# Kernel optimization log

Measured on AMD Instinct MI355X. Metric: run time of the kernel, lower is better.

The kernel has to match this reference:

```python
import jax, jax.numpy as jnp
import numpy as np

B, S, D, E, H, TOPK = 4, 2048, 1024, 32, 128, 4

def setup_inputs() -> dict:
    key = jax.random.key(0)
    k1, k2, k3, k4 = jax.random.split(key, 4)
    x = jax.random.normal(k1, (B, S, D), jnp.float32)
    expert_sel = jax.random.normal(k2, (E, D), jnp.float32) * (D ** -0.5)
    keys = jax.random.normal(k3, (E, D, H), jnp.float32) * (D ** -0.5)
    values = jax.random.normal(k4, (E, H, D), jnp.float32) * (H ** -0.5)
    return {"x": x, "expert_sel": expert_sel, "keys": keys, "values": values, "n_heads": TOPK}

def reference(x, expert_sel, keys, values, n_heads):
    # x: [B,S,D]; expert_sel: [E,D]; keys: [E,D,H]; values: [E,H,D]
    Bv, Sv, Dv = x.shape
    Ev = keys.shape[0]
    xf = x.reshape(-1, Dv)                                  # [N,D]
    N = xf.shape[0]
    gate = jax.nn.sigmoid(xf @ expert_sel.T)                # [N,E] sigmoid gating (sigma-MoE)
    vals, idx = jax.lax.top_k(gate, n_heads)                # [N,k] selected experts + gate weights
    # dense per-token-per-expert gate weights; zero for non-selected experts
    g = jnp.zeros((N, Ev), x.dtype).at[jnp.arange(N)[:, None], idx].set(vals)  # [N,E]
    # grouped expert FFN, expressed densely over the (small) expert axis:
    # out = sum_e g[n,e] * relu(x @ keys[e]) @ values[e]
    h = jax.nn.relu(jnp.einsum('nd,edh->enh', xf, keys))    # [E,N,H]
    out = jnp.einsum('enh,ehd->nd', h * g.T[:, :, None], values)  # [N,D]
    return out.reshape(Bv, Sv, Dv)
```

## Files before the change

### kernel.cpp

```cpp
#include <hip/hip_runtime.h>
#include <hip/hip_bf16.h>

#define NTOK 8192
#define DDIM 1024
#define NEXP 32
#define HDIM 128
#define TOPK 4

typedef __attribute__((ext_vector_type(8))) short bf16x8;
typedef __attribute__((ext_vector_type(4))) float f32x4;

typedef unsigned int uint_g __attribute__((address_space(1)));
typedef unsigned int uint_l __attribute__((address_space(3)));

__device__ __forceinline__ void async_cp16(const void* g, void* l) {
    __builtin_amdgcn_global_load_lds((const uint_g*)g, (uint_l*)l, 16, 0, 0);
}

__device__ inline unsigned short f2bf(float f) {
    unsigned int u = __builtin_bit_cast(unsigned int, f);
    unsigned int r = (u + 0x7fffu + ((u >> 16) & 1u)) >> 16;
    return (unsigned short)r;
}
__device__ inline float bf2f(unsigned short s) {
    unsigned int u = ((unsigned int)s) << 16;
    return __builtin_bit_cast(float, u);
}

__global__ __launch_bounds__(256) void prep_gate(
    const float* __restrict__ x, const float* __restrict__ es,
    const float* __restrict__ keys, const float* __restrict__ values,
    unsigned short* __restrict__ Kb, unsigned short* __restrict__ Vb,
    unsigned short* __restrict__ Xb,
    int* __restrict__ cnt, int* __restrict__ tok_list, float* __restrict__ gates)
{
    const int tid = threadIdx.x;

    if (blockIdx.x >= 512) {
        int idx = (int)(blockIdx.x - 512) * 256 + tid;
        unsigned short o[8];
        if (idx < NEXP * 128 * 128) {
            int n = idx & 127, k0 = (idx >> 7) & 127, e = idx >> 14;
            const float* s = keys + ((size_t)e * DDIM + k0 * 8) * HDIM + n;
            #pragma unroll
            for (int j = 0; j < 8; ++j) o[j] = f2bf(s[(size_t)j * HDIM]);
            *(uint4*)&Kb[(size_t)idx * 8] = *(uint4*)o;
        } else {
            idx -= NEXP * 128 * 128;
            int n = idx & 1023, k0 = (idx >> 10) & 15, e = idx >> 14;
            const float* s = values + ((size_t)e * HDIM + k0 * 8) * DDIM + n;
            #pragma unroll
            for (int j = 0; j < 8; ++j) o[j] = f2bf(s[(size_t)j * DDIM]);
            *(uint4*)&Vb[(size_t)idx * 8] = *(uint4*)o;
        }
        return;
    }

    const int n0 = (int)blockIdx.x * 16;

    __shared__ float smem[4608];
    __shared__ float Ls[16 * 33];
    __shared__ int hist[NEXP];
    __shared__ int bbase[NEXP];
    float* Xt  = smem;
    float* Est = smem + 64 * 36;
    float* Lp  = smem;

    const int t4  = (tid & 3) * 4;
    const int e4  = ((tid >> 2) & 7) * 4;
    const int rep = tid >> 5;

    const int xr = tid & 15, xc4 = (tid >> 4) * 4;
    const int er = tid & 31, ec8 = (tid >> 5) * 8;

    const int ctok = tid >> 4, cd4 = (tid & 15) * 4;

    const int rtok = tid >> 5, re = tid & 31;

    float lsum[2] = {0.f, 0.f};

    if (tid < NEXP) hist[tid] = 0;

    float4 xv  = *(const float4*)&x[(size_t)(n0 + xr) * DDIM + xc4];
    float4 ev0 = *(const float4*)&es[(size_t)er * DDIM + ec8];
    float4 ev1 = *(const float4*)&es[(size_t)er * DDIM + ec8 + 4];

    for (int q = 0; q < 4; ++q) {
        float acc[4][4] = {};

        for (int dci = 0; dci < 4; ++dci) {
            const int dc = q * 256 + dci * 64;
            __syncthreads();
            {
                Xt[(xc4 + 0) * 36 + xr] = xv.x; Xt[(xc4 + 1) * 36 + xr] = xv.y;
                Xt[(xc4 + 2) * 36 + xr] = xv.z; Xt[(xc4 + 3) * 36 + xr] = xv.w;
                Est[(ec8 + 0) * 36 + er] = ev0.x; Est[(ec8 + 1) * 36 + er] = ev0.y;
                Est[(ec8 + 2) * 36 + er] = ev0.z; Est[(ec8 + 3) * 36 + er] = ev0.w;
                Est[(ec8 + 4) * 36 + er] = ev1.x; Est[(ec8 + 5) * 36 + er] = ev1.y;
                Est[(ec8 + 6) * 36 + er] = ev1.z; Est[(ec8 + 7) * 36 + er] = ev1.w;
            }
            const int nxt = dc + 64;
            if (nxt < DDIM) {
                xv  = *(const float4*)&x[(size_t)(n0 + xr) * DDIM + nxt + xc4];
                ev0 = *(const float4*)&es[(size_t)er * DDIM + nxt + ec8];
                ev1 = *(const float4*)&es[(size_t)er * DDIM + nxt + ec8 + 4];
            }
            __syncthreads();

            {
                unsigned short o[4];
                #pragma unroll
                for (int j = 0; j < 4; ++j) o[j] = f2bf(Xt[(cd4 + j) * 36 + ctok]);
                *(uint2*)&Xb[(size_t)(n0 + ctok) * DDIM + dc + cd4] = *(uint2*)o;
            }

            #pragma unroll
            for (int s = 0; s < 8; ++s) {
                int d = s * 8 + rep;
                float4 xa4 = *(const float4*)&Xt[d * 36 + t4];
                float4 ea4 = *(const float4*)&Est[d * 36 + e4];
                const float xa[4] = {xa4.x, xa4.y, xa4.z, xa4.w};
                const float ea[4] = {ea4.x, ea4.y, ea4.z, ea4.w};
                #pragma unroll
                for (int i = 0; i < 4; ++i)
                    #pragma unroll
                    for (int j = 0; j < 4; ++j)
                        acc[i][j] = fmaf(xa[i], ea[j], acc[i][j]);
            }
        }

        __syncthreads();
        #pragma unroll
        for (int i = 0; i < 4; ++i)
            #pragma unroll
            for (int j = 0; j < 4; ++j)
                Lp[(rep * 16 + t4 + i) * 33 + e4 + j] = acc[i][j];
        __syncthreads();

        #pragma unroll
        for (int h = 0; h < 2; ++h) {
            int tok = rtok + h * 8;
            float s = 0.f;
            #pragma unroll
            for (int r = 0; r < 8; ++r) s += Lp[(r * 16 + tok) * 33 + re];
            lsum[h] += s;
        }
    }

    #pragma unroll
    for (int h = 0; h < 2; ++h) Ls[(rtok + h * 8) * 33 + re] = lsum[h];
    __syncthreads();

    int sel[TOPK]; int lpos[TOPK];
    if (tid < 16) {
        float lg[NEXP];
        #pragma unroll
        for (int e2 = 0; e2 < NEXP; ++e2) lg[e2] = Ls[tid * 33 + e2];
        float sv[TOPK];
        #pragma unroll
        for (int j = 0; j < TOPK; ++j) {
            float bv = -3.0e38f; int bi = 0;
            #pragma unroll
            for (int e2 = 0; e2 < NEXP; ++e2) {
                bool taken = false;
                #pragma unroll
                for (int qq = 0; qq < j; ++qq) taken = taken || (sel[qq] == e2);
                float v = taken ? -3.0e38f : lg[e2];
                if (v > bv) { bv = v; bi = e2; }
            }
            sel[j] = bi; sv[j] = bv;
        }
        #pragma unroll
        for (int j = 0; j < TOPK; ++j) {
            gates[(size_t)(n0 + tid) * TOPK + j] = 1.f / (1.f + expf(-sv[j]));
            lpos[j] = atomicAdd(&hist[sel[j]], 1);
        }
    }
    __syncthreads();
    if (tid < NEXP) bbase[tid] = atomicAdd(&cnt[tid], hist[tid]);
    __syncthreads();
    if (tid < 16) {
        #pragma unroll
        for (int j = 0; j < TOPK; ++j)
            tok_list[(size_t)sel[j] * NTOK + bbase[sel[j]] + lpos[j]] = (n0 + tid) * TOPK + j;
    }
}

__global__ __launch_bounds__(256) void ffn_fused(
    const unsigned short* __restrict__ Xb,
    const unsigned short* __restrict__ Kb,
    const unsigned short* __restrict__ Vb,
    const int* __restrict__ cnt, const int* __restrict__ tok_list,
    const float* __restrict__ gates,
    unsigned short* __restrict__ Ob)
{
    const int bid = blockIdx.x;
    const int e = bid & 31, tile = bid >> 5;
    const int c = cnt[e], base = tile * 32;
    if (base >= c) return;
    const int nt   = min(32, c - base);
    const int tid  = threadIdx.x, wave = tid >> 6, lane = tid & 63;
    const int lm   = lane & 15, quad = lane >> 4;
    const int r2   = (wave >> 1) * 16;
    const int c2   = (wave & 1) * 64;
    const int cw   = (wave & 1) * 32;

    __shared__ __align__(16) unsigned short KV[8192];
    __shared__ __align__(16) unsigned short XO[2304];
    __shared__ __align__(16) unsigned short Hs[32 * 140];
    __shared__ int slot[32]; __shared__ int gtok[32]; __shared__ float gs[32];

    if (tid < 32) {
        if (tid < nt) {
            int v = tok_list[(size_t)e * NTOK + base + tid];
            slot[tid] = v; gtok[tid] = v >> 2; gs[tid] = gates[v];
        } else { slot[tid] = -1; gtok[tid] = 0; gs[tid] = 0.f; }
    }
    __syncthreads();

    const unsigned short* Ke = Kb + (size_t)e * 131072;
    const unsigned short* Ve = Vb + (size_t)e * 131072;
    const unsigned short* xrowb = Xb + (size_t)gtok[lane & 31] * DDIM + (lane >> 5) * 8;

    f32x4 acc[4];
    #pragma unroll
    for (int j = 0; j < 4; ++j) acc[j] = (f32x4){0.f, 0.f, 0.f, 0.f};

    auto stageA = [&](int t) {
        int dc = t * 64;
        #pragma unroll
        for (int i = 0; i < 4; ++i) {
            int p = wave * 4 + i;
            async_cp16(Ke + ((size_t)(dc / 8 + (p >> 1)) * 128 + (p & 1) * 64 + lane) * 8,
                       &KV[p * 512]);
        }
        async_cp16(xrowb + dc + wave * 16, &XO[wave * 512]);
    };

    stageA(0);
    __syncthreads();

    for (int t = 0; t < 16; ++t) {
        #pragma unroll
        for (int ks = 0; ks < 2; ++ks) {
            int k0 = ks * 4 + quad;
            bf16x8 a0 = *(const bf16x8*)&XO[(k0 * 32 + r2 + lm) * 8];
            #pragma unroll
            for (int tj = 0; tj < 4; ++tj) {
                bf16x8 bb = *(const bf16x8*)&KV[(k0 * 128 + c2 + tj * 16 + lm) * 8];
                acc[tj] = __builtin_amdgcn_mfma_f32_16x16x32_bf16(a0, bb, acc[tj], 0, 0, 0);
            }
        }
        if (t < 15) {
            __syncthreads();
            stageA(t + 1);
            __syncthreads();
        }
    }

    #pragma unroll
    for (int reg = 0; reg < 4; ++reg) {
        int m = r2 + quad * 4 + reg;
        float g = gs[m];
        #pragma unroll
        for (int tj = 0; tj < 4; ++tj)
            Hs[m * 140 + c2 + tj * 16 + lm] = f2bf(fmaxf(acc[tj][reg], 0.f) * g);
    }
    __syncthreads();

    auto stageV = [&](int cc) {
        #pragma unroll
        for (int i = 0; i < 4; ++i) {
            int p = wave * 4 + i;
            async_cp16(Ve + ((size_t)p * 1024 + cc * 64 + lane) * 8, &KV[p * 512]);
        }
    };

    stageV(0);
    __syncthreads();

    bf16x8 hf[4];
    #pragma unroll
    for (int ks = 0; ks < 4; ++ks)
        hf[ks] = *(const bf16x8*)&Hs[(r2 + lm) * 140 + (ks * 4 + quad) * 8];

    const int om = tid >> 3, oq = tid & 7;
    const int os = slot[om];

    for (int cc = 0; cc < 16; ++cc) {
        f32x4 acc2[2];
        acc2[0] = (f32x4){0.f, 0.f, 0.f, 0.f};
        acc2[1] = (f32x4){0.f, 0.f, 0.f, 0.f};

        #pragma unroll
        for (int ks = 0; ks < 4; ++ks) {
            int k0 = ks * 4 + quad;
            #pragma unroll
            for (int tj = 0; tj < 2; ++tj) {
                bf16x8 bb = *(const bf16x8*)&KV[(k0 * 64 + cw + tj * 16 + lm) * 8];
                acc2[tj] = __builtin_amdgcn_mfma_f32_16x16x32_bf16(hf[ks], bb, acc2[tj], 0, 0, 0);
            }
        }

        #pragma unroll
        for (int reg = 0; reg < 4; ++reg) {
            int m = r2 + quad * 4 + reg;
            XO[m * 72 + cw + lm]      = f2bf(acc2[0][reg]);
            XO[m * 72 + cw + 16 + lm] = f2bf(acc2[1][reg]);
        }
        __syncthreads();

        if (os >= 0) {
            uint4 v0 = *(const uint4*)&XO[om * 72 + oq * 8];
            *(uint4*)(Ob + (size_t)os * DDIM + cc * 64 + oq * 8) = v0;
        }
        if (cc < 15) stageV(cc + 1);
        __syncthreads();
    }
}

__global__ __launch_bounds__(256) void reduce_out(
    const unsigned short* __restrict__ Ob, float* __restrict__ out)
{
    const int tid = threadIdx.x;
    const int n   = blockIdx.x * 2 + (tid >> 7);
    const int cc  = (tid & 127) * 8;

    float s[8] = {};
    #pragma unroll
    for (int j = 0; j < 4; ++j) {
        uint4 v = *(const uint4*)&Ob[((size_t)n * 4 + j) * DDIM + cc];
        const unsigned int w[4] = {v.x, v.y, v.z, v.w};
        #pragma unroll
        for (int q = 0; q < 4; ++q) {
            s[q * 2 + 0] += bf2f((unsigned short)(w[q] & 0xffff));
            s[q * 2 + 1] += bf2f((unsigned short)(w[q] >> 16));
        }
    }
    float4 o0 = {s[0], s[1], s[2], s[3]};
    float4 o1 = {s[4], s[5], s[6], s[7]};
    *(float4*)&out[(size_t)n * DDIM + cc]     = o0;
    *(float4*)&out[(size_t)n * DDIM + cc + 4] = o1;
}

extern "C" void kernel_launch(void* const* d_in, const int* in_sizes, int n_in,
                              void* d_out, int out_size, void* d_ws, size_t ws_size,
                              hipStream_t stream) {
    const float* x      = (const float*)d_in[0];
    const float* es     = (const float*)d_in[1];
    const float* keys   = (const float*)d_in[2];
    const float* values = (const float*)d_in[3];
    float* out          = (float*)d_out;

    char* w = (char*)d_ws;
    int*   cnt      = (int*)w;               w += 256;
    int*   tok_list = (int*)w;               w += (size_t)NEXP * NTOK * sizeof(int);
    float* gates    = (float*)w;             w += (size_t)NTOK * TOPK * sizeof(float);
    unsigned short* Kb = (unsigned short*)w; w += (size_t)NEXP * 128 * 128 * 8 * 2;
    unsigned short* Vb = (unsigned short*)w; w += (size_t)NEXP * 16 * 1024 * 8 * 2;
    unsigned short* Xb = (unsigned short*)w; w += (size_t)NTOK * DDIM * 2;
    unsigned short* Ob = (unsigned short*)w;

    hipMemsetAsync(cnt, 0, NEXP * sizeof(int), stream);

    prep_gate<<<512 + 4096, 256, 0, stream>>>(x, es, keys, values, Kb, Vb, Xb,
                                              cnt, tok_list, gates);
    ffn_fused<<<256 * NEXP, 256, 0, stream>>>(Xb, Kb, Vb, cnt, tok_list, gates, Ob);
    reduce_out<<<NTOK / 2, 256, 0, stream>>>(Ob, out);
}
```

Baseline: 197.1 us.

## Double-buffer K/V tiles in LDS and load X rows directly into registers

The K and V weight tiles now go into two LDS buffers, with prefetch issued two steps ahead. This drops one of the two barriers per iteration in both GEMM loops. X activations are read straight from global memory into registers with one-step prefetch instead of being staged through LDS. The output staging buffer is also double-buffered so the next tile's writes do not race the global stores. The aim is to overlap global loads with MFMA work, at the cost of roughly doubling LDS usage, which may reduce how many blocks fit per CU.

```diff
diff --git a/kernel.cpp b/kernel.cpp
--- a/kernel.cpp
+++ b/kernel.cpp
@@ -205,9 +205,9 @@
     const int c2   = (wave & 1) * 64;
     const int cw   = (wave & 1) * 32;
 
-    __shared__ __align__(16) unsigned short KV[8192];
-    __shared__ __align__(16) unsigned short XO[2304];
+    __shared__ __align__(16) unsigned short KV[2][8192];
     __shared__ __align__(16) unsigned short Hs[32 * 140];
+    __shared__ __align__(16) unsigned short OSB[2][2304];
     __shared__ int slot[32]; __shared__ int gtok[32]; __shared__ float gs[32];
 
     if (tid < 32) {
@@ -220,44 +220,58 @@
 
     const unsigned short* Ke = Kb + (size_t)e * 131072;
     const unsigned short* Ve = Vb + (size_t)e * 131072;
-    const unsigned short* xrowb = Xb + (size_t)gtok[lane & 31] * DDIM + (lane >> 5) * 8;
-
-    f32x4 acc[4];
-    #pragma unroll
-    for (int j = 0; j < 4; ++j) acc[j] = (f32x4){0.f, 0.f, 0.f, 0.f};
-
-    auto stageA = [&](int t) {
-        int dc = t * 64;
+    const unsigned short* xp = Xb + (size_t)gtok[r2 + lm] * DDIM + quad * 8;
+
+    auto stageK = [&](int t, int cb) {
         #pragma unroll
         for (int i = 0; i < 4; ++i) {
             int p = wave * 4 + i;
-            async_cp16(Ke + ((size_t)(dc / 8 + (p >> 1)) * 128 + (p & 1) * 64 + lane) * 8,
-                       &KV[p * 512]);
-        }
-        async_cp16(xrowb + dc + wave * 16, &XO[wave * 512]);
+            async_cp16(Ke + ((size_t)(t * 8 + (p >> 1)) * 128 + (p & 1) * 64 + lane) * 8,
+                       &KV[cb][p * 512]);
+        }
     };
-
-    stageA(0);
+    auto stageV = [&](int cc, int vb) {
+        #pragma unroll
+        for (int i = 0; i < 4; ++i) {
+            int p = wave * 4 + i;
+            async_cp16(Ve + ((size_t)p * 1024 + cc * 64 + lane) * 8, &KV[vb][p * 512]);
+        }
+    };
+
+    f32x4 acc[4];
+    #pragma unroll
+    for (int j = 0; j < 4; ++j) acc[j] = (f32x4){0.f, 0.f, 0.f, 0.f};
+
+    stageK(0, 0);
+    stageK(1, 1);
+    bf16x8 xc0 = *(const bf16x8*)&xp[0];
+    bf16x8 xc1 = *(const bf16x8*)&xp[32];
     __syncthreads();
 
     for (int t = 0; t < 16; ++t) {
+        bf16x8 xn0, xn1;
+        if (t < 15) {
+            xn0 = *(const bf16x8*)&xp[(t + 1) * 64];
+            xn1 = *(const bf16x8*)&xp[(t + 1) * 64 + 32];
+        }
+        const unsigned short* B = KV[t & 1];
         #pragma unroll
         for (int ks = 0; ks < 2; ++ks) {
             int k0 = ks * 4 + quad;
-            bf16x8 a0 = *(const bf16x8*)&XO[(k0 * 32 + r2 + lm) * 8];
+            bf16x8 a0 = ks ? xc1 : xc0;
             #pragma unroll
             for (int tj = 0; tj < 4; ++tj) {
-                bf16x8 bb = *(const bf16x8*)&KV[(k0 * 128 + c2 + tj * 16 + lm) * 8];
+                bf16x8 bb = *(const bf16x8*)&B[(k0 * 128 + c2 + tj * 16 + lm) * 8];
                 acc[tj] = __builtin_amdgcn_mfma_f32_16x16x32_bf16(a0, bb, acc[tj], 0, 0, 0);
             }
         }
-        if (t < 15) {
-            __syncthreads();
-            stageA(t + 1);
-            __syncthreads();
-        }
-    }
-
+        __syncthreads();
+        if (t + 2 < 16) stageK(t + 2, t & 1);
+        xc0 = xn0; xc1 = xn1;
+    }
+
+    stageV(0, 0);
+    stageV(1, 1);
     #pragma unroll
     for (int reg = 0; reg < 4; ++reg) {
         int m = r2 + quad * 4 + reg;
@@ -268,17 +282,6 @@
     }
     __syncthreads();
 
-    auto stageV = [&](int cc) {
-        #pragma unroll
-        for (int i = 0; i < 4; ++i) {
-            int p = wave * 4 + i;
-            async_cp16(Ve + ((size_t)p * 1024 + cc * 64 + lane) * 8, &KV[p * 512]);
-        }
-    };
-
-    stageV(0);
-    __syncthreads();
-
     bf16x8 hf[4];
     #pragma unroll
     for (int ks = 0; ks < 4; ++ks)
@@ -288,6 +291,7 @@
     const int os = slot[om];
 
     for (int cc = 0; cc < 16; ++cc) {
+        const int p = cc & 1;
         f32x4 acc2[2];
         acc2[0] = (f32x4){0.f, 0.f, 0.f, 0.f};
         acc2[1] = (f32x4){0.f, 0.f, 0.f, 0.f};
@@ -297,7 +301,7 @@
             int k0 = ks * 4 + quad;
             #pragma unroll
             for (int tj = 0; tj < 2; ++tj) {
-                bf16x8 bb = *(const bf16x8*)&KV[(k0 * 64 + cw + tj * 16 + lm) * 8];
+                bf16x8 bb = *(const bf16x8*)&KV[p][(k0 * 64 + cw + tj * 16 + lm) * 8];
                 acc2[tj] = __builtin_amdgcn_mfma_f32_16x16x32_bf16(hf[ks], bb, acc2[tj], 0, 0, 0);
             }
         }
@@ -305,17 +309,16 @@
         #pragma unroll
         for (int reg = 0; reg < 4; ++reg) {
             int m = r2 + quad * 4 + reg;
-            XO[m * 72 + cw + lm]      = f2bf(acc2[0][reg]);
-            XO[m * 72 + cw + 16 + lm] = f2bf(acc2[1][reg]);
+            OSB[p][m * 72 + cw + lm]      = f2bf(acc2[0][reg]);
+            OSB[p][m * 72 + cw + 16 + lm] = f2bf(acc2[1][reg]);
         }
         __syncthreads();
+        if (cc + 2 < 16) stageV(cc + 2, p);
 
         if (os >= 0) {
-            uint4 v0 = *(const uint4*)&XO[om * 72 + oq * 8];
+            uint4 v0 = *(const uint4*)&OSB[p][om * 72 + oq * 8];
             *(uint4*)(Ob + (size_t)os * DDIM + cc * 64 + oq * 8) = v0;
         }
-        if (cc < 15) stageV(cc + 1);
-        __syncthreads();
     }
 }
 
```

New measurement: 210.1 us. 1.07x slower.
